# Optimization experiments

Measured on AMD Instinct MI355X. Metric: run time of the kernel, lower is better.

Reference implementation:

```python
import jax, jax.numpy as jnp
import numpy as np

N_NODES = 100_000
N_EDGES = 6_400_000
CH = 5


def setup_inputs() -> dict:
    key = jax.random.key(0)
    ks = jax.random.split(key, 16)
    inp = {
        "x": jax.random.normal(ks[0], (N_NODES, 2), dtype=jnp.float32),
        "edge_index": jax.random.randint(ks[1], (2, N_EDGES), 0, N_NODES, dtype=jnp.int64 if jax.config.jax_enable_x64 else jnp.int32).astype(jnp.int32),
        "edge_attr": jax.random.uniform(ks[2], (N_EDGES, 1), dtype=jnp.float32),
        "lin1_w": jax.random.normal(ks[3], (2, CH), dtype=jnp.float32) * 0.5,
        "lin1_b": jax.random.normal(ks[4], (CH,), dtype=jnp.float32) * 0.1,
        "conv1_wf": jax.random.normal(ks[5], (2 * CH + 1, CH), dtype=jnp.float32) * 0.3,
        "conv1_bf": jax.random.normal(ks[6], (CH,), dtype=jnp.float32) * 0.1,
        "conv1_ws": jax.random.normal(ks[7], (2 * CH + 1, CH), dtype=jnp.float32) * 0.3,
        "conv1_bs": jax.random.normal(ks[8], (CH,), dtype=jnp.float32) * 0.1,
        "conv2_wf": jax.random.normal(ks[9], (2 * CH + 1, CH), dtype=jnp.float32) * 0.3,
        "conv2_bf": jax.random.normal(ks[10], (CH,), dtype=jnp.float32) * 0.1,
        "conv2_ws": jax.random.normal(ks[11], (2 * CH + 1, CH), dtype=jnp.float32) * 0.3,
        "conv2_bs": jax.random.normal(ks[12], (CH,), dtype=jnp.float32) * 0.1,
        "lin2_w": jax.random.normal(ks[13], (CH, 2), dtype=jnp.float32) * 0.5,
        "lin2_b": jax.random.normal(ks[14], (2,), dtype=jnp.float32) * 0.1,
    }
    return inp


def cgconv(x, edge_index, edge_attr, wf, bf, ws, bs):
    # PyG CGConv: x_i' = x_i + sum_{j->i} sigmoid(z W_f + b_f) * softplus(z W_s + b_s)
    # z = [x_i, x_j, e_ij]; edge_index[0]=source j, edge_index[1]=target i
    src, dst = edge_index[0], edge_index[1]
    z = jnp.concatenate([x[dst], x[src], edge_attr], axis=-1)  # [E, 2C+dim]
    msg = jax.nn.sigmoid(z @ wf + bf) * jax.nn.softplus(z @ ws + bs)  # [E, C]
    agg = jax.ops.segment_sum(msg, dst, num_segments=x.shape[0])  # [N, C]
    return x + agg


def reference(x, edge_index, edge_attr,
              lin1_w, lin1_b,
              conv1_wf, conv1_bf, conv1_ws, conv1_bs,
              conv2_wf, conv2_bf, conv2_ws, conv2_bs,
              lin2_w, lin2_b):
    h = x @ lin1_w + lin1_b  # [N, C]
    h = cgconv(h, edge_index, edge_attr, conv1_wf, conv1_bf, conv1_ws, conv1_bs)
    h = cgconv(h, edge_index, edge_attr, conv2_wf, conv2_bf, conv2_ws, conv2_bs)
    return h @ lin2_w + lin2_b  # [N, 2]
```

## Files before the change

### kernel.cpp

```cpp
#include <hip/hip_runtime.h>
#include <hip/hip_fp16.h>

constexpr int NN = 100000;
constexpr int NE = 6400000;
constexpr int BSH = 7;
constexpr int BN = 1 << BSH;
constexpr int NBUCK = (NN + BN - 1) / BN;
constexpr int BCAP = 9216;
constexpr int STILE = 4096;
constexpr int NSB = (NE + STILE - 1) / STILE;
constexpr int NP = 1024;

#define LOG2E 1.44269504f
#define LN2   0.69314718f


__global__ __launch_bounds__(256) void k_lin2(const float* __restrict__ h,
                                              const float* __restrict__ w,
                                              const float* __restrict__ b,
                                              float* __restrict__ out) {
    int n = blockIdx.x * 256 + threadIdx.x;
    if (n >= NN) return;
    float o0 = b[0], o1 = b[1];
#pragma unroll
    for (int c = 0; c < 5; ++c) {
        float hv = h[(size_t)n * 5 + c];
        o0 += hv * w[2 * c];
        o1 += hv * w[2 * c + 1];
    }
    out[2 * n] = o0;
    out[2 * n + 1] = o1;
}

__device__ __forceinline__ void prep_core(const float hv[5],
                                          const float* __restrict__ wf,
                                          const float* __restrict__ bf,
                                          const float* __restrict__ ws,
                                          const float* __restrict__ bs,
                                          int n, float* __restrict__ TD,
                                          unsigned short* __restrict__ TSh) {
    float tg[5], ts[5], sg[5], ss[5];
#pragma unroll
    for (int c = 0; c < 5; ++c) {
        float a = bf[c], d = bs[c], u = 0.f, v = 0.f;
#pragma unroll
        for (int k = 0; k < 5; ++k) {
            a += hv[k] * wf[k * 5 + c];
            d += hv[k] * ws[k * 5 + c];
            u += hv[k] * wf[(5 + k) * 5 + c];
            v += hv[k] * ws[(5 + k) * 5 + c];
        }
        tg[c] = -a * LOG2E; ts[c] = -d * LOG2E;
        sg[c] = -u * LOG2E; ss[c] = -v * LOG2E;
    }
    float4* Dp = (float4*)(TD + (size_t)n * 12);
    Dp[0] = make_float4(tg[0], tg[1], tg[2], tg[3]);
    Dp[1] = make_float4(tg[4], ts[0], ts[1], ts[2]);
    Dp[2] = make_float4(ts[3], ts[4], 0.f, 0.f);

    unsigned p[5];
#pragma unroll
    for (int c = 0; c < 5; ++c) {
        unsigned lo = (unsigned)__half_as_ushort(__float2half_rn(sg[c]));
        unsigned hi = (unsigned)__half_as_ushort(__float2half_rn(ss[c]));
        p[c] = lo | (hi << 16);
    }
    uint4 w0 = make_uint4(p[0], p[1], p[2], p[3]);
    uint4 w1 = make_uint4(p[4], 0u, 0u, 0u);
    *(uint4*)(TSh + (size_t)n * 16) = w0;
    *(uint4*)(TSh + (size_t)n * 16 + 8) = w1;
}

__global__ __launch_bounds__(256) void k_prep1(const float* __restrict__ x,
                                               const float* __restrict__ l1w,
                                               const float* __restrict__ l1b,
                                               const float* __restrict__ wf,
                                               const float* __restrict__ bf,
                                               const float* __restrict__ ws,
                                               const float* __restrict__ bs,
                                               float* __restrict__ TD,
                                               unsigned short* __restrict__ TSh,
                                               float* __restrict__ h) {
    int n = blockIdx.x * 256 + threadIdx.x;
    if (n >= NN) return;
    float x0 = x[2 * n], x1 = x[2 * n + 1];
    float hv[5];
#pragma unroll
    for (int c = 0; c < 5; ++c) {
        hv[c] = l1b[c] + x0 * l1w[c] + x1 * l1w[5 + c];
        h[(size_t)n * 5 + c] = hv[c];
    }
    prep_core(hv, wf, bf, ws, bs, n, TD, TSh);
}

__global__ __launch_bounds__(256) void k_prep(const float* __restrict__ h,
                                              const float* __restrict__ wf,
                                              const float* __restrict__ bf,
                                              const float* __restrict__ ws,
                                              const float* __restrict__ bs,
                                              float* __restrict__ TD,
                                              unsigned short* __restrict__ TSh) {
    int n = blockIdx.x * 256 + threadIdx.x;
    if (n >= NN) return;
    float hv[5];
#pragma unroll
    for (int k = 0; k < 5; ++k) hv[k] = h[(size_t)n * 5 + k];
    prep_core(hv, wf, bf, ws, bs, n, TD, TSh);
}

__global__ __launch_bounds__(256) void k_initcurs(int* __restrict__ gcurs) {
    int i = blockIdx.x * 256 + threadIdx.x;
    if (i < NBUCK) gcurs[i] = i * BCAP;
}

__global__ __launch_bounds__(512) void k_scatter5(const int* __restrict__ ei,
                                                  const float* __restrict__ ea,
                                                  int* __restrict__ gcurs,
                                                  unsigned int* __restrict__ rec) {
    __shared__ unsigned int lrec[STILE];
    __shared__ unsigned short lbkt[STILE];
    __shared__ unsigned short spk[STILE];
    __shared__ int C[NBUCK];
    __shared__ int loc[NBUCK];
    __shared__ int gbase[NBUCK];
    __shared__ int A[NP];
    __shared__ int wsum[16];
    const int tid = threadIdx.x, blk = blockIdx.x;
    const int base = blk * STILE;
    const int m = min(STILE, NE - base);

    for (int i = tid; i < NBUCK; i += 512) C[i] = 0;
    __syncthreads();

    const int m4 = m >> 2;
    const int4* s4 = (const int4*)(ei + base);
    const int4* d4 = (const int4*)(ei + NE + base);
    const float4* a4 = (const float4*)(ea + base);
    for (int q = tid; q < m4; q += 512) {
        int4 s = s4[q];
        int4 d = d4[q];
        float4 a = a4[q];
        int k = q * 4;
        lrec[k + 0] = (unsigned)s.x | ((unsigned)(d.x & (BN - 1)) << 17) |
                      (__float2uint_rn(a.x * 255.f) << 24);
        lrec[k + 1] = (unsigned)s.y | ((unsigned)(d.y & (BN - 1)) << 17) |
                      (__float2uint_rn(a.y * 255.f) << 24);
        lrec[k + 2] = (unsigned)s.z | ((unsigned)(d.z & (BN - 1)) << 17) |
                      (__float2uint_rn(a.z * 255.f) << 24);
        lrec[k + 3] = (unsigned)s.w | ((unsigned)(d.w & (BN - 1)) << 17) |
                      (__float2uint_rn(a.w * 255.f) << 24);
        lbkt[k + 0] = (unsigned short)((unsigned)d.x >> BSH);
        lbkt[k + 1] = (unsigned short)((unsigned)d.y >> BSH);
        lbkt[k + 2] = (unsigned short)((unsigned)d.z >> BSH);
        lbkt[k + 3] = (unsigned short)((unsigned)d.w >> BSH);
        atomicAdd(&C[(unsigned)d.x >> BSH], 1);
        atomicAdd(&C[(unsigned)d.y >> BSH], 1);
        atomicAdd(&C[(unsigned)d.z >> BSH], 1);
        atomicAdd(&C[(unsigned)d.w >> BSH], 1);
    }
    __syncthreads();

    for (int b = tid; b < NBUCK; b += 512)
        gbase[b] = C[b] ? atomicAdd(&gcurs[b], C[b]) : 0;

    const int lane = tid & 63;
    const int wv = tid >> 6;
    int orig[2], incl[2];
#pragma unroll
    for (int half = 0; half < 2; ++half) {
        int c = wv + half * 8;
        int i = c * 64 + lane;
        int v = (i < NBUCK) ? C[i] : 0;
        orig[half] = v;
#pragma unroll
        for (int off = 1; off < 64; off <<= 1) {
            int t = __shfl_up(v, off, 64);
            if (lane >= off) v += t;
        }
        incl[half] = v;
        if (lane == 63) wsum[c] = v;
    }
    __syncthreads();
    if (tid < 16) {
        int v = wsum[tid];
#pragma unroll
        for (int off = 1; off < 16; off <<= 1) {
            int t = __shfl_up(v, off, 16);
            if (tid >= off) v += t;
        }
        wsum[tid] = v;
    }
    __syncthreads();
#pragma unroll
    for (int half = 0; half < 2; ++half) {
        int c = wv + half * 8;
        int i = c * 64 + lane;
        int coff = (c > 0) ? wsum[c - 1] : 0;
        int excl = incl[half] - orig[half] + coff;
        A[i] = excl;
        if (i < NBUCK) loc[i] = excl;
    }
    __syncthreads();

    for (int k = tid; k < m; k += 512) {
        int bkt = lbkt[k];
        int p = atomicAdd(&loc[bkt], 1);
        spk[p] = (unsigned short)k;
    }
    __syncthreads();

    for (int p = tid; p < m; p += 512) {
        int k = spk[p];
        int bkt = lbkt[k];
        rec[gbase[bkt] + (p - A[bkt])] = lrec[k];
    }
}

__global__ __launch_bounds__(512) void k_sortbkt(const int* __restrict__ gcurs,
                                                 unsigned int* __restrict__ rec,
                                                 int2* __restrict__ nrange) {
    __shared__ unsigned int lrec[BCAP];
    __shared__ int cnt[BN];
    __shared__ int curs[BN];
    const int b = blockIdx.x, tid = threadIdx.x;
    const int e0 = b * BCAP;
    const int m = gcurs[b] - e0;
    const int node0 = b << BSH;
    const int nloc = min(BN, NN - node0);

    for (int i = tid; i < m; i += 512) lrec[i] = rec[e0 + i];
    if (tid < BN) cnt[tid] = 0;
    __syncthreads();
    for (int i = tid; i < m; i += 512)
        atomicAdd(&cnt[(lrec[i] >> 17) & (BN - 1)], 1);
    __syncthreads();
    int v = (tid < BN) ? cnt[tid] : 0;
    for (int off = 1; off < BN; off <<= 1) {
        int t = 0;
        if (tid < BN && tid >= off) t = cnt[tid - off];
        __syncthreads();
        if (tid < BN) cnt[tid] += t;
        __syncthreads();
    }
    if (tid < BN) {
        int excl = cnt[tid] - v;
        curs[tid] = excl;
        if (tid < nloc)
            nrange[node0 + tid] = make_int2(e0 + excl, e0 + excl + v);
    }
    __syncthreads();
    for (int i = tid; i < m; i += 512) {
        unsigned int r = lrec[i];
        int dl = (r >> 17) & (BN - 1);
        int pos = atomicAdd(&curs[dl], 1);
        rec[e0 + pos] = r;
    }
}

__global__ __launch_bounds__(256) void k_conv_csr(
        const unsigned int* __restrict__ rec, const int2* __restrict__ nrange,
        const float* __restrict__ TD, const unsigned short* __restrict__ TSh,
        const float* __restrict__ wf, const float* __restrict__ ws,
        float* __restrict__ h ) {
    const int tid = threadIdx.x;
    const int lane = tid & 15;
    const int n = blockIdx.x * 16 + (tid >> 4);

    __half2 we2[5];
#pragma unroll
    for (int c = 0; c < 5; ++c)
        we2[c] = __floats2half2_rn(-wf[50 + c] * LOG2E, -ws[50 + c] * LOG2E);

    const float4* Dp = (const float4*)(TD + (size_t)n * 12);
    float4 d0 = Dp[0], d1 = Dp[1], d2 = Dp[2];
    const float Tg[5] = {d0.x, d0.y, d0.z, d0.w, d1.x};
    const float Ts[5] = {d1.y, d1.z, d1.w, d2.x, d2.y};
    __half2 dd2[5];
#pragma unroll
    for (int c = 0; c < 5; ++c) dd2[c] = __floats2half2_rn(Tg[c], Ts[c]);

    const __half2 one2 = __float2half2_rn(1.f);
    const __half hz = __float2half(0.f);

    float acc[5] = {0.f, 0.f, 0.f, 0.f, 0.f};
    const int2 rg = nrange[n];
    const int eEnd = rg.y;
    for (int e = rg.x + lane; e < eEnd; e += 64) {
        unsigned r[4];
        bool vld[4];
        float4 q0[4];
        unsigned q1[4];
        __half2 a2[4];
#pragma unroll
        for (int j = 0; j < 4; ++j) {
            int ej = e + j * 16;
            vld[j] = ej < eEnd;
            r[j] = rec[vld[j] ? ej : e];
        }
#pragma unroll
        for (int j = 0; j < 4; ++j) {
            const unsigned src = r[j] & 0x1FFFFu;
            const unsigned short* row = TSh + (size_t)src * 16;
            q0[j] = *(const float4*)row;
            q1[j] = *(const unsigned*)(row + 8);
            a2[j] = __float2half2_rn((float)(r[j] >> 24) * (1.f / 255.f));
        }
#pragma unroll
        for (int j = 0; j < 4; ++j) {
            if (!vld[j]) continue;
            union { float4 f; __half2 h2[4]; } u; u.f = q0[j];
            __half2 s2[5] = {u.h2[0], u.h2[1], u.h2[2], u.h2[3],
                             *(__half2*)&q1[j]};
#pragma unroll
            for (int c = 0; c < 5; ++c) {
                __half2 z2 = __hadd2(__hfma2(a2[j], we2[c], dd2[c]), s2[c]);
                __half zx = __low2half(z2);
                __half zy = __high2half(z2);
                __half nab = __hmin(zy, __hneg(zy));
                __half2 e2 = h2exp2(__halves2half2(zx, nab));
                __half2 o2 = __hadd2(e2, one2);
                float sig = __half2float(hrcp(__low2half(o2)));
                float lg  = __half2float(hlog2(__high2half(o2)));
                float mx  = __half2float(__hmin(zy, hz));
                acc[c] = fmaf(sig, lg - mx, acc[c]);
            }
        }
    }
#pragma unroll
    for (int off = 8; off >= 1; off >>= 1)
#pragma unroll
        for (int c = 0; c < 5; ++c)
            acc[c] += __shfl_xor(acc[c], off, 16);
    if (lane == 0) {
#pragma unroll
        for (int c = 0; c < 5; ++c)
            h[(size_t)n * 5 + c] += LN2 * acc[c];
    }
}

__global__ __launch_bounds__(256) void k_prep_fb(const float* __restrict__ h,
                                                 const float* __restrict__ wf,
                                                 const float* __restrict__ bf,
                                                 const float* __restrict__ ws,
                                                 const float* __restrict__ bs,
                                                 float* __restrict__ T,
                                                 float* __restrict__ S,
                                                 float* __restrict__ hout) {
    int n = blockIdx.x * 256 + threadIdx.x;
    if (n >= NN) return;
    float hv[5];
#pragma unroll
    for (int k = 0; k < 5; ++k) hv[k] = h[5 * n + k];
    float tf[5], ts[5], sf[5], ss[5];
#pragma unroll
    for (int c = 0; c < 5; ++c) {
        float a = bf[c], d = bs[c], u = 0.f, v = 0.f;
#pragma unroll
        for (int k = 0; k < 5; ++k) {
            a += hv[k] * wf[k * 5 + c];
            d += hv[k] * ws[k * 5 + c];
            u += hv[k] * wf[(5 + k) * 5 + c];
            v += hv[k] * ws[(5 + k) * 5 + c];
        }
        tf[c] = a; ts[c] = d; sf[c] = u; ss[c] = v;
    }
    float4* Tp = (float4*)(T + (size_t)n * 16);
    Tp[0] = make_float4(tf[0], tf[1], tf[2], tf[3]);
    Tp[1] = make_float4(tf[4], ts[0], ts[1], ts[2]);
    Tp[2] = make_float4(ts[3], ts[4], 0.f, 0.f);
    float4* Sp = (float4*)(S + (size_t)n * 16);
    Sp[0] = make_float4(sf[0], sf[1], sf[2], sf[3]);
    Sp[1] = make_float4(sf[4], ss[0], ss[1], ss[2]);
    Sp[2] = make_float4(ss[3], ss[4], 0.f, 0.f);
#pragma unroll
    for (int c = 0; c < 5; ++c) hout[5 * n + c] = hv[c];
}

__global__ __launch_bounds__(256) void k_conv_atomic(const int* __restrict__ ei,
                                                     const float* __restrict__ ea,
                                                     const float* __restrict__ T,
                                                     const float* __restrict__ S,
                                                     const float* __restrict__ wf,
                                                     const float* __restrict__ ws,
                                                     float* __restrict__ hout) {
    int e = blockIdx.x * 256 + threadIdx.x;
    if (e >= NE) return;
    int src = ei[e];
    int dst = ei[NE + e];
    float a = ea[e];
    const float4* Tp = (const float4*)(T + (size_t)dst * 16);
    const float4* Sp = (const float4*)(S + (size_t)src * 16);
    float4 t0 = Tp[0], t1 = Tp[1], t2 = Tp[2];
    float4 s0 = Sp[0], s1 = Sp[1], s2 = Sp[2];
    float za[5] = {t0.x + s0.x, t0.y + s0.y, t0.z + s0.z, t0.w + s0.w, t1.x + s1.x};
    float zs[5] = {t1.y + s1.y, t1.z + s1.z, t1.w + s1.w, t2.x + s2.x, t2.y + s2.y};
    float* outp = hout + (size_t)dst * 5;
#pragma unroll
    for (int c = 0; c < 5; ++c) {
        float f = za[c] + a * wf[50 + c];
        float s = zs[c] + a * ws[50 + c];
        float sig = 1.f / (1.f + __expf(-f));
        float sp = __logf(1.f + __expf(-fabsf(s))) + fmaxf(s, 0.f);
        unsafeAtomicAdd(outp + c, sig * sp);
    }
}

__global__ __launch_bounds__(256) void k_lin1_fb(const float* __restrict__ x,
                                                 const float* __restrict__ w,
                                                 const float* __restrict__ b,
                                                 float* __restrict__ h) {
    int n = blockIdx.x * 256 + threadIdx.x;
    if (n >= NN) return;
    float x0 = x[2 * n], x1 = x[2 * n + 1];
#pragma unroll
    for (int c = 0; c < 5; ++c)
        h[5 * n + c] = b[c] + x0 * w[c] + x1 * w[5 + c];
}

extern "C" void kernel_launch(void* const* d_in, const int* in_sizes, int n_in,
                              void* d_out, int out_size, void* d_ws, size_t ws_size,
                              hipStream_t stream) {
    const float* x    = (const float*)d_in[0];
    const int*   ei   = (const int*)d_in[1];
    const float* ea   = (const float*)d_in[2];
    const float* l1w  = (const float*)d_in[3];
    const float* l1b  = (const float*)d_in[4];
    const float* c1wf = (const float*)d_in[5];
    const float* c1bf = (const float*)d_in[6];
    const float* c1ws = (const float*)d_in[7];
    const float* c1bs = (const float*)d_in[8];
    const float* c2wf = (const float*)d_in[9];
    const float* c2bf = (const float*)d_in[10];
    const float* c2ws = (const float*)d_in[11];
    const float* c2bs = (const float*)d_in[12];
    const float* l2w  = (const float*)d_in[13];
    const float* l2b  = (const float*)d_in[14];
    float* out = (float*)d_out;
    char* ws = (char*)d_ws;

    size_t o_rec    = 0;
    size_t o_nrange = o_rec + (size_t)NBUCK * BCAP * 4;
    size_t o_gcurs  = o_nrange + (size_t)NN * 8;
    size_t o_TD     = (o_gcurs + (size_t)NBUCK * 4 + 15) & ~(size_t)15;
    size_t o_TS     = o_TD + (size_t)NN * 12 * 4;
    size_t o_h      = o_TS + (size_t)NN * 16 * 2;
    size_t need     = o_h + (size_t)NN * 5 * 4;

    int nb_n = (NN + 255) / 256;

    if (ws_size >= need) {
        unsigned int* rec    = (unsigned int*)(ws + o_rec);
        int2* nrange         = (int2*)(ws + o_nrange);
        int* gcurs           = (int*)(ws + o_gcurs);
        float* TD            = (float*)(ws + o_TD);
        unsigned short* TSh  = (unsigned short*)(ws + o_TS);
        float* h             = (float*)(ws + o_h);

        k_initcurs<<<(NBUCK + 255) / 256, 256, 0, stream>>>(gcurs);
        k_scatter5<<<NSB,   512, 0, stream>>>(ei, ea, gcurs, rec);
        k_sortbkt <<<NBUCK, 512, 0, stream>>>(gcurs, rec, nrange);

        k_prep1<<<nb_n, 256, 0, stream>>>(x, l1w, l1b,
                                          c1wf, c1bf, c1ws, c1bs, TD, TSh, h);
        k_conv_csr<<<NN / 16, 256, 0, stream>>>(rec, nrange, TD, TSh,
                                                c1wf, c1ws, h);
        k_prep<<<nb_n, 256, 0, stream>>>(h, c2wf, c2bf, c2ws, c2bs, TD, TSh);
        k_conv_csr<<<NN / 16, 256, 0, stream>>>(rec, nrange, TD, TSh,
                                                c2wf, c2ws, h);
        k_lin2<<<nb_n, 256, 0, stream>>>(h, l2w, l2b, out);
    } else {
        float* h0 = (float*)(ws);
        float* h1 = (float*)(ws + 2000000);
        float* h2 = h0;
        float* T  = (float*)(ws + 4000000);
        float* S  = (float*)(ws + 10400000);
        int nb_e = (NE + 255) / 256;

        k_lin1_fb<<<nb_n, 256, 0, stream>>>(x, l1w, l1b, h0);
        k_prep_fb<<<nb_n, 256, 0, stream>>>(h0, c1wf, c1bf, c1ws, c1bs, T, S, h1);
        k_conv_atomic<<<nb_e, 256, 0, stream>>>(ei, ea, T, S, c1wf, c1ws, h1);
        k_prep_fb<<<nb_n, 256, 0, stream>>>(h1, c2wf, c2bf, c2ws, c2bs, T, S, h2);
        k_conv_atomic<<<nb_e, 256, 0, stream>>>(ei, ea, T, S, c2wf, c2ws, h2);
        k_lin2<<<nb_n, 256, 0, stream>>>(h2, l2w, l2b, out);
    }
}
```

Before: 200.0 us.

## Replace atomic bucket cursors with count/scan pass for compact edge bucketing

```diff
diff --git a/kernel.cpp b/kernel.cpp
--- a/kernel.cpp
+++ b/kernel.cpp
@@ -7,7 +7,7 @@
 constexpr int BN = 1 << BSH;
 constexpr int NBUCK = (NN + BN - 1) / BN;
 constexpr int BCAP = 9216;
-constexpr int STILE = 4096;
+constexpr int STILE = 8192;
 constexpr int NSB = (NE + STILE - 1) / STILE;
 constexpr int NP = 1024;
 
@@ -108,14 +108,90 @@
     prep_core(hv, wf, bf, ws, bs, n, TD, TSh);
 }
 
-__global__ __launch_bounds__(256) void k_initcurs(int* __restrict__ gcurs) {
-    int i = blockIdx.x * 256 + threadIdx.x;
-    if (i < NBUCK) gcurs[i] = i * BCAP;
-}
-
-__global__ __launch_bounds__(512) void k_scatter5(const int* __restrict__ ei,
+__global__ __launch_bounds__(512) void k_count(const int* __restrict__ ei,
+                                               int* __restrict__ counts) {
+    __shared__ int hist[NBUCK];
+    const int tid = threadIdx.x, blk = blockIdx.x;
+    for (int i = tid; i < NBUCK; i += 512) hist[i] = 0;
+    __syncthreads();
+    const int base = blk * STILE;
+    const int m = min(STILE, NE - base);
+    for (int k = tid; k < m; k += 512)
+        atomicAdd(&hist[(unsigned)ei[NE + base + k] >> BSH], 1);
+    __syncthreads();
+    for (int i = tid; i < NBUCK; i += 512)
+        counts[(size_t)i * NSB + blk] = hist[i];
+}
+
+__global__ __launch_bounds__(256) void k_rowsum(const int* __restrict__ counts,
+                                                int* __restrict__ total) {
+    __shared__ int red[256];
+    const int b = blockIdx.x, tid = threadIdx.x;
+    int s = 0;
+    for (int i = tid; i < NSB; i += 256) s += counts[(size_t)b * NSB + i];
+    red[tid] = s;
+    __syncthreads();
+    for (int o = 128; o > 0; o >>= 1) {
+        if (tid < o) red[tid] += red[tid + o];
+        __syncthreads();
+    }
+    if (tid == 0) total[b] = red[0];
+}
+
+__global__ __launch_bounds__(256) void k_scan(const int* __restrict__ in,
+                                              int* __restrict__ bstart, int L) {
+    __shared__ int buf[256];
+    const int tid = threadIdx.x;
+    int carry = 0;
+    for (int c0 = 0; c0 < L; c0 += 256) {
+        int i = c0 + tid;
+        int v = (i < L) ? in[i] : 0;
+        buf[tid] = v;
+        __syncthreads();
+        for (int off = 1; off < 256; off <<= 1) {
+            int t = (tid >= off) ? buf[tid - off] : 0;
+            __syncthreads();
+            buf[tid] += t;
+            __syncthreads();
+        }
+        int incl = buf[tid];
+        int chunk_total = buf[255];
+        if (i < L) bstart[i] = carry + incl - v;
+        carry += chunk_total;
+        __syncthreads();
+    }
+    if (tid == 0) bstart[L] = carry;
+}
+
+__global__ __launch_bounds__(256) void k_rowoffs(const int* __restrict__ counts,
+                                                 const int* __restrict__ bstart,
+                                                 int* __restrict__ offsT) {
+    __shared__ int buf[256];
+    const int b = blockIdx.x, tid = threadIdx.x;
+    int carry = bstart[b];
+    const int* row = counts + (size_t)b * NSB;
+    for (int c0 = 0; c0 < NSB; c0 += 256) {
+        int i = c0 + tid;
+        int v = (i < NSB) ? row[i] : 0;
+        buf[tid] = v;
+        __syncthreads();
+        for (int off = 1; off < 256; off <<= 1) {
+            int t = (tid >= off) ? buf[tid - off] : 0;
+            __syncthreads();
+            buf[tid] += t;
+            __syncthreads();
+        }
+        int incl = buf[tid];
+        int chunk_total = buf[255];
+        if (i < NSB) offsT[(size_t)i * NBUCK + b] = carry + incl - v;
+        carry += chunk_total;
+        __syncthreads();
+    }
+}
+
+__global__ __launch_bounds__(512) void k_scatter6(const int* __restrict__ ei,
                                                   const float* __restrict__ ea,
-                                                  int* __restrict__ gcurs,
+                                                  const int* __restrict__ offsT,
                                                   unsigned int* __restrict__ rec) {
     __shared__ unsigned int lrec[STILE];
     __shared__ unsigned short lbkt[STILE];
@@ -160,8 +236,8 @@
     }
     __syncthreads();
 
-    for (int b = tid; b < NBUCK; b += 512)
-        gbase[b] = C[b] ? atomicAdd(&gcurs[b], C[b]) : 0;
+    const int* orow = offsT + (size_t)blk * NBUCK;
+    for (int b = tid; b < NBUCK; b += 512) gbase[b] = orow[b];
 
     const int lane = tid & 63;
     const int wv = tid >> 6;
@@ -216,15 +292,15 @@
     }
 }
 
-__global__ __launch_bounds__(512) void k_sortbkt(const int* __restrict__ gcurs,
+__global__ __launch_bounds__(512) void k_sortbkt(const int* __restrict__ bstart,
                                                  unsigned int* __restrict__ rec,
                                                  int2* __restrict__ nrange) {
     __shared__ unsigned int lrec[BCAP];
     __shared__ int cnt[BN];
     __shared__ int curs[BN];
     const int b = blockIdx.x, tid = threadIdx.x;
-    const int e0 = b * BCAP;
-    const int m = gcurs[b] - e0;
+    const int e0 = bstart[b];
+    const int m = bstart[b + 1] - e0;
     const int node0 = b << BSH;
     const int nloc = min(BN, NN - node0);
 
@@ -439,9 +515,12 @@
     char* ws = (char*)d_ws;
 
     size_t o_rec    = 0;
-    size_t o_nrange = o_rec + (size_t)NBUCK * BCAP * 4;
-    size_t o_gcurs  = o_nrange + (size_t)NN * 8;
-    size_t o_TD     = (o_gcurs + (size_t)NBUCK * 4 + 15) & ~(size_t)15;
+    size_t o_nrange = o_rec + (size_t)NE * 4;
+    size_t o_counts = o_nrange + (size_t)NN * 8;
+    size_t o_offsT  = o_counts + (size_t)NBUCK * NSB * 4;
+    size_t o_total  = o_offsT + (size_t)NSB * NBUCK * 4;
+    size_t o_bstart = o_total + (size_t)NBUCK * 4;
+    size_t o_TD     = (o_bstart + (size_t)(NBUCK + 1) * 4 + 15) & ~(size_t)15;
     size_t o_TS     = o_TD + (size_t)NN * 12 * 4;
     size_t o_h      = o_TS + (size_t)NN * 16 * 2;
     size_t need     = o_h + (size_t)NN * 5 * 4;
@@ -451,14 +530,20 @@
     if (ws_size >= need) {
         unsigned int* rec    = (unsigned int*)(ws + o_rec);
         int2* nrange         = (int2*)(ws + o_nrange);
-        int* gcurs           = (int*)(ws + o_gcurs);
+        int* counts          = (int*)(ws + o_counts);
+        int* offsT           = (int*)(ws + o_offsT);
+        int* total           = (int*)(ws + o_total);
+        int* bstart          = (int*)(ws + o_bstart);
         float* TD            = (float*)(ws + o_TD);
         unsigned short* TSh  = (unsigned short*)(ws + o_TS);
         float* h             = (float*)(ws + o_h);
 
-        k_initcurs<<<(NBUCK + 255) / 256, 256, 0, stream>>>(gcurs);
-        k_scatter5<<<NSB,   512, 0, stream>>>(ei, ea, gcurs, rec);
-        k_sortbkt <<<NBUCK, 512, 0, stream>>>(gcurs, rec, nrange);
+        k_count   <<<NSB,   512, 0, stream>>>(ei, counts);
+        k_rowsum  <<<NBUCK, 256, 0, stream>>>(counts, total);
+        k_scan    <<<1,     256, 0, stream>>>(total, bstart, NBUCK);
+        k_rowoffs <<<NBUCK, 256, 0, stream>>>(counts, bstart, offsT);
+        k_scatter6<<<NSB,   512, 0, stream>>>(ei, ea, offsT, rec);
+        k_sortbkt <<<NBUCK, 512, 0, stream>>>(bstart, rec, nrange);
 
         k_prep1<<<nb_n, 256, 0, stream>>>(x, l1w, l1b,
                                           c1wf, c1bf, c1ws, c1bs, TD, TSh, h);
```

After: 209.3 us. 4.6% more time.
